# Optimization experiments

Hardware: AMD Instinct MI355X
Metric: run time of the kernel (lower is better)

## Reference

```python
import jax, jax.numpy as jnp
import numpy as np

N = 200_000           # particles
E = 6_400_000         # neighbor pairs (~32 per particle)
SUPPORT = 0.05
EPS = SUPPORT ** 2 * 0.1
DELTA = 0.1
C0 = 10.0 * float(np.sqrt(2.0 * 9.81 * 0.3))
REST_DENSITY = 1000.0
_KC = 7.0 / float(np.pi)  # 2D Wendland C2 normalization


def kernel_gradient(q, dirs, h):
    # Wendland C2 (2D): W = C/h^2 (1-q)^4 (1+4q), q = r/h in [0,1]
    # dW/dr = C/h^3 * (-20 q (1-q)^3), directed along unit vector dirs
    dkdq = -20.0 * q * (1.0 - q) ** 3 * _KC
    return dirs * (dkdq / h ** 3)[:, None]


def setup_inputs() -> dict:
    key = jax.random.key(0)
    k = jax.random.split(key, 7)
    i = jnp.sort(jax.random.randint(k[0], (E,), 0, N))
    j = jax.random.randint(k[1], (E,), 0, N)
    fluidPosition = jax.random.uniform(k[2], (N, 2), dtype=jnp.float32)
    dx2 = (SUPPORT * 0.5) ** 2
    fluidVolume = dx2 * (1.0 + 0.01 * jax.random.normal(k[3], (N,), dtype=jnp.float32))
    fluidDensity = 0.95 + 0.1 * jax.random.uniform(k[4], (N,), dtype=jnp.float32)
    d = jax.random.normal(k[5], (E, 2), dtype=jnp.float32)
    distances = d / (jnp.linalg.norm(d, axis=1, keepdims=True) + 1e-8)  # unit directions
    radialDistances = jax.random.uniform(k[6], (E,), dtype=jnp.float32, minval=0.05, maxval=1.0)
    return {"fluidPosition": fluidPosition, "fluidVolume": fluidVolume,
            "fluidDensity": fluidDensity, "distances": distances,
            "radialDistances": radialDistances, "i": i, "j": j}


def reference(fluidPosition, fluidVolume, fluidDensity, distances, radialDistances, i, j):
    h = SUPPORT
    n = fluidDensity.shape[0]
    gradW = kernel_gradient(radialDistances, distances, h)          # [E,2]
    r_ba = -distances * (radialDistances * h)[:, None]              # [E,2] displacement
    Vj = fluidVolume[j]

    # --- normalization matrix: sum_j 2 Vj * outer(r_ba, gradW) ---
    term = jnp.einsum('nu,nv->nuv', r_ba, gradW) * (2.0 * Vj)[:, None, None]
    M = jax.ops.segment_sum(term, i, num_segments=n)                # [N,2,2]

    # --- pseudo-inverse + renormalized kernel gradient per edge ---
    Li = jnp.linalg.pinv(M)                                         # [N,2,2]
    grad = jnp.einsum('nuv,nv->nu', Li[i], gradW)                   # [E,2]
    dwij_mag = jnp.sum(jnp.abs(gradW), axis=1)                      # L1 norms
    norm_mag = jnp.sum(jnp.abs(grad), axis=1)
    change = jnp.abs(norm_mag - dwij_mag) / (dwij_mag + 1e-4 * h)
    grad = jnp.where((change < 0.1)[:, None], grad, gradW)

    # --- renormalized density gradient ---
    rho = fluidDensity * REST_DENSITY
    rho_ba = rho[j] - rho[i]
    gradRho = jax.ops.segment_sum((2.0 * rho_ba * Vj)[:, None] * grad, i, num_segments=n)

    # --- deltaSPH density diffusion ---
    rji2 = jnp.sum(r_ba * r_ba, axis=1) + EPS
    densityTerm = 0.5 * jnp.einsum('nu,nu->n', gradRho[i] + gradRho[j], r_ba)
    gradTerm = jnp.einsum('nu,nu->n', gradW, r_ba / rji2[:, None])
    prod = (rho_ba + densityTerm) * gradTerm
    return 2.0 * h * DELTA * C0 * jax.ops.segment_sum(prod * Vj, i, num_segments=n)
```

## Files before the change

### kernel.cpp

```cpp
#include <hip/hip_runtime.h>
#include <hip/hip_fp16.h>
#include <math.h>

#define WAVE   64
#define NPB    32
#define BLOCKT 256
#define SMAX   2

#define KC        2.2281692032865347f
#define H         0.05f
#define INV_H2    400.0f
#define INV_H3    8000.0f
#define EPS_REF   0.00025f
#define K_OUT     0.24261080f
#define REST_RHO  1000.0f

__device__ __forceinline__ float wendland_dkdq(float q) {
    float o = 1.f - q;
    return -20.f * q * o * o * o * KC;
}

union H2F { __half2 h; float f; };
__device__ __forceinline__ float   h2_as_f(__half2 h) { H2F u; u.h = h; return u.f; }
__device__ __forceinline__ __half2 f_as_h2(float f)   { H2F u; u.f = f; return u.h; }

__device__ __forceinline__ int li_search(const int* rp, int e) {
    int lo = 0;
#pragma unroll
    for (int s = NPB / 2; s >= 1; s >>= 1) lo += (rp[lo + s] <= e) ? s : 0;
    return lo;
}

template<int NV>
__device__ __forceinline__ void seg_reduce4(const int k[4], float v[4][NV], float* base) {
    const int lane = threadIdx.x & (WAVE - 1);
    const int k0 = k[0], k3 = k[3];
    const bool split = (k0 != k3);
    const int firstLen  = (k[1]==k0) ? ((k[2]==k0) ? ((k[3]==k0)?4:3) : 2) : 1;
    const int lastStart = (k[2]==k3) ? ((k[1]==k3) ? ((k[0]==k3)?0:1) : 2) : 3;

    float vin[NV], vfirst[NV];
#pragma unroll
    for (int c = 0; c < NV; ++c) {
        float s = v[3][c];
        if (lastStart <= 2) s += v[2][c];
        if (lastStart <= 1) s += v[1][c];
        if (lastStart == 0) s += v[0][c];
        vin[c] = s;
        float f = v[0][c];
        if (firstLen >= 2) f += v[1][c];
        if (firstLen >= 3) f += v[2][c];
        if (firstLen >= 4) f += v[3][c];
        vfirst[c] = f;
    }
#pragma unroll
    for (int idx = 1; idx <= 2; ++idx) {
        if (idx >= firstLen && idx < lastStart && k[idx] >= 0) {
#pragma unroll
            for (int c = 0; c < NV; ++c)
                atomicAdd(base + (size_t)k[idx] * NV + c, v[idx][c]);
        }
    }
    float S[NV];
#pragma unroll
    for (int c = 0; c < NV; ++c) S[c] = vin[c];
    const int klast = k3;
#pragma unroll
    for (int d = 1; d < WAVE; d <<= 1) {
        int okey = __shfl_up(klast, d, WAVE);
        float ov[NV];
#pragma unroll
        for (int c = 0; c < NV; ++c) ov[c] = __shfl_up(S[c], d, WAVE);
        if (lane >= d && okey == klast) {
#pragma unroll
            for (int c = 0; c < NV; ++c) S[c] += ov[c];
        }
    }
    const int prevk = __shfl_up(klast, 1, WAVE);
    float P[NV];
#pragma unroll
    for (int c = 0; c < NV; ++c) P[c] = __shfl_up(S[c], 1, WAVE);
    if (split && k0 >= 0) {
        const bool carry = (lane > 0 && prevk == k0);
#pragma unroll
        for (int c = 0; c < NV; ++c)
            atomicAdd(base + (size_t)k0 * NV + c, vfirst[c] + (carry ? P[c] : 0.f));
    }
    const int nk0 = __shfl_down(k0, 1, WAVE);
    const bool tail = (lane == WAVE - 1) || (nk0 != klast);
    if (tail && klast >= 0) {
#pragma unroll
        for (int c = 0; c < NV; ++c)
            atomicAdd(base + (size_t)klast * NV + c, S[c]);
    }
}

struct EW { int jv[4]; float qv[4], dxv[4], dyv[4]; bool okv[4]; };

__device__ __forceinline__ void load_win(long e0, int beg, int end, int E,
        const int* __restrict__ ej, const float* __restrict__ qarr,
        const float2* __restrict__ dirs, EW& w) {
    if (e0 + 3 < (long)E) {
        int4   j4 = *(const int4*)(ej + e0);
        float4 q4 = *(const float4*)(qarr + e0);
        float4 dA = *(const float4*)((const float*)dirs + 2 * e0);
        float4 dB = *(const float4*)((const float*)dirs + 2 * e0 + 4);
        w.jv[0]=j4.x; w.jv[1]=j4.y; w.jv[2]=j4.z; w.jv[3]=j4.w;
        w.qv[0]=q4.x; w.qv[1]=q4.y; w.qv[2]=q4.z; w.qv[3]=q4.w;
        w.dxv[0]=dA.x; w.dyv[0]=dA.y; w.dxv[1]=dA.z; w.dyv[1]=dA.w;
        w.dxv[2]=dB.x; w.dyv[2]=dB.y; w.dxv[3]=dB.z; w.dyv[3]=dB.w;
    } else {
#pragma unroll
        for (int u = 0; u < 4; ++u) {
            long e = e0 + u;
            if (e < (long)E) {
                w.jv[u] = ej[e]; w.qv[u] = qarr[e];
                float2 d = dirs[e]; w.dxv[u] = d.x; w.dyv[u] = d.y;
            } else { w.jv[u]=0; w.qv[u]=0.f; w.dxv[u]=0.f; w.dyv[u]=0.f; }
        }
    }
#pragma unroll
    for (int u = 0; u < 4; ++u) {
        long e = e0 + u;
        w.okv[u] = (e >= (long)beg) && (e < (long)end);
    }
}

__global__ void k_prep(const int* __restrict__ ei, const float* __restrict__ vol,
                       const float* __restrict__ dens, int* __restrict__ rowptr,
                       float2* __restrict__ vd, int N, int E) {
    int e = blockIdx.x * blockDim.x + threadIdx.x;
    if (e <= E) {
        int prev = (e == 0) ? -1 : ei[e - 1];
        int cur  = (e == E) ? N  : ei[e];
        for (int t = prev + 1; t <= cur; ++t) rowptr[t] = e;
    }
    if (e < N) vd[e] = make_float2(vol[e], dens[e]);
}

__global__ __launch_bounds__(BLOCKT, 4)
void k_AC(const int* __restrict__ ej, const float* __restrict__ qarr,
          const float2* __restrict__ dirs, const float2* __restrict__ vd,
          const int* __restrict__ rowptr, __half2* __restrict__ cst,
          float2* __restrict__ g2, float* __restrict__ outp, int N, int E) {
    __shared__ int    rp[NPB + 1];
    __shared__ float  acc6[NPB * 6];
    __shared__ float  Lild[NPB * 3];
    __shared__ float  gld[NPB * 2];
    __shared__ float2 vdl[NPB];
    const int tid = threadIdx.x;
    const int n0  = blockIdx.x * NPB;
    const int nHi = min(n0 + NPB, N);
    if (tid <= NPB) rp[tid] = rowptr[min(n0 + tid, nHi)];
    if (tid < NPB && n0 + tid < N) vdl[tid] = vd[n0 + tid];
    if (tid < NPB * 6) acc6[tid] = 0.f;
    if (tid < NPB * 2) gld[tid] = 0.f;
    __syncthreads();
    const int  beg = rp[0], end = rp[NPB];
    const long beg4 = (long)beg & ~3L;
    const int  waveBase = tid & ~(WAVE - 1);

    int   li_s[4 * SMAX];
    float w_s[4 * SMAX], dx_s[4 * SMAX], dy_s[4 * SMAX], val_s[4 * SMAX];
#pragma unroll
    for (int x = 0; x < 4 * SMAX; ++x) { li_s[x] = -1; w_s[x]=dx_s[x]=dy_s[x]=val_s[x]=0.f; }

#pragma unroll
    for (int c = 0; c < SMAX; ++c) {
        long ebw = beg4 + ((long)c * BLOCKT + waveBase) * 4;
        if (ebw < (long)end) {
            long e0 = beg4 + ((long)c * BLOCKT + tid) * 4;
            EW wd; load_win(e0, beg, end, E, ej, qarr, dirs, wd);
            const bool all4 = wd.okv[0] && wd.okv[1] && wd.okv[2] && wd.okv[3];
            float4 cpack;
            int k[4]; float v[4][6];
#pragma unroll
            for (int u = 0; u < 4; ++u) {
                k[u] = -1;
#pragma unroll
                for (int c2 = 0; c2 < 6; ++c2) v[u][c2] = 0.f;
                if (wd.okv[u]) {
                    int li = li_search(rp, (int)(e0 + u));
                    float q = wd.qv[u], dx = wd.dxv[u], dy = wd.dyv[u];
                    float2 vdj = vd[wd.jv[u]];
                    float wq = wendland_dkdq(q);
                    float s = -2.f * vdj.x * q * wq * INV_H2;
                    float w = wq * INV_H3;
                    float gwx = dx * w, gwy = dy * w;
                    float rx = -dx * q * H, ry = -dy * q * H;
                    float rji2 = rx * rx + ry * ry + EPS_REF;
                    float gT = (gwx * rx + gwy * ry) / rji2;
                    float gv = gT * vdj.x;
                    float rho_ba = REST_RHO * (vdj.y - vdl[li].y);
                    k[u] = li;
                    v[u][0] = s * dx * dx; v[u][1] = s * dx * dy; v[u][2] = s * dy * dy;
                    v[u][3] = rho_ba * gv; v[u][4] = rx * gv;    v[u][5] = ry * gv;
                    __half2 cp = __floats2half2_rn(0.5f * rx * gv, 0.5f * ry * gv);
                    if (all4) (&cpack.x)[u] = h2_as_f(cp);
                    else      cst[e0 + u] = cp;
                    li_s[c*4+u] = li; w_s[c*4+u] = w;
                    dx_s[c*4+u] = dx; dy_s[c*4+u] = dy;
                    val_s[c*4+u] = 2.f * rho_ba * vdj.x;
                }
            }
            if (all4) ((float4*)cst)[e0 >> 2] = cpack;
            seg_reduce4<6>(k, v, acc6);
        }
    }
    for (int c = SMAX; ; ++c) {
        long ebw = beg4 + ((long)c * BLOCKT + waveBase) * 4;
        if (ebw >= (long)end) break;
        long e0 = beg4 + ((long)c * BLOCKT + tid) * 4;
        EW wd; load_win(e0, beg, end, E, ej, qarr, dirs, wd);
        int k[4]; float v[4][6];
#pragma unroll
        for (int u = 0; u < 4; ++u) {
            k[u] = -1;
#pragma unroll
            for (int c2 = 0; c2 < 6; ++c2) v[u][c2] = 0.f;
            if (wd.okv[u]) {
                int li = li_search(rp, (int)(e0 + u));
                float q = wd.qv[u], dx = wd.dxv[u], dy = wd.dyv[u];
                float2 vdj = vd[wd.jv[u]];
                float wq = wendland_dkdq(q);
                float s = -2.f * vdj.x * q * wq * INV_H2;
                float w = wq * INV_H3;
                float gwx = dx * w, gwy = dy * w;
                float rx = -dx * q * H, ry = -dy * q * H;
                float rji2 = rx * rx + ry * ry + EPS_REF;
                float gT = (gwx * rx + gwy * ry) / rji2;
                float gv = gT * vdj.x;
                float rho_ba = REST_RHO * (vdj.y - vdl[li].y);
                k[u] = li;
                v[u][0] = s * dx * dx; v[u][1] = s * dx * dy; v[u][2] = s * dy * dy;
                v[u][3] = rho_ba * gv; v[u][4] = rx * gv;    v[u][5] = ry * gv;
                cst[e0 + u] = __floats2half2_rn(0.5f * rx * gv, 0.5f * ry * gv);
            }
        }
        seg_reduce4<6>(k, v, acc6);
    }
    __syncthreads();

    if (tid < NPB) {
        float a = acc6[6*tid], b = acc6[6*tid+1], cc = acc6[6*tid+2];
        float half_tr   = 0.5f * (a + cc);
        float half_diff = 0.5f * (a - cc);
        float disc = sqrtf(half_diff * half_diff + b * b);
        float l1 = half_tr + disc, l2 = half_tr - disc;
        float smax = fmaxf(fabsf(l1), fabsf(l2));
        float cutoff = 2.3841858e-6f * smax;
        float i00 = 0.f, i01 = 0.f, i11 = 0.f;
        if (fabsf(l2) > cutoff) {
            float inv = 1.0f / (a * cc - b * b);
            i00 =  cc * inv; i01 = -b * inv; i11 = a * inv;
        } else if (fabsf(l1) > cutoff) {
            float vax = b,       vay = l1 - a;
            float vbx = l1 - cc, vby = b;
            float na = vax*vax + vay*vay, nb = vbx*vbx + vby*vby;
            float vx, vy, n2;
            if (nb >= na) { vx = vbx; vy = vby; n2 = nb; }
            else          { vx = vax; vy = vay; n2 = na; }
            float inv = 1.0f / (l1 * n2);
            i00 = vx*vx*inv; i01 = vx*vy*inv; i11 = vy*vy*inv;
        }
        Lild[3*tid] = i00; Lild[3*tid+1] = i01; Lild[3*tid+2] = i11;
    }
    __syncthreads();

#pragma unroll
    for (int c = 0; c < SMAX; ++c) {
        long ebw = beg4 + ((long)c * BLOCKT + waveBase) * 4;
        if (ebw < (long)end) {
            int k[4]; float v[4][2];
#pragma unroll
            for (int u = 0; u < 4; ++u) {
                int li = li_s[c*4+u];
                k[u] = li; v[u][0] = v[u][1] = 0.f;
                if (li >= 0) {
                    float w = w_s[c*4+u], dx = dx_s[c*4+u], dy = dy_s[c*4+u];
                    float gwx = dx * w, gwy = dy * w;
                    float L0 = Lild[3*li], L1 = Lild[3*li+1], L2v = Lild[3*li+2];
                    float gx = L0 * gwx + L1 * gwy;
                    float gy = L1 * gwx + L2v * gwy;
                    float dm = fabsf(gwx) + fabsf(gwy);
                    float nm = fabsf(gx) + fabsf(gy);
                    float change = fabsf(nm - dm) / (dm + 1e-4f * H);
                    if (!(change < 0.1f)) { gx = gwx; gy = gwy; }
                    v[u][0] = val_s[c*4+u] * gx;
                    v[u][1] = val_s[c*4+u] * gy;
                }
            }
            seg_reduce4<2>(k, v, gld);
        }
    }
    for (int c = SMAX; ; ++c) {
        long ebw = beg4 + ((long)c * BLOCKT + waveBase) * 4;
        if (ebw >= (long)end) break;
        long e0 = beg4 + ((long)c * BLOCKT + tid) * 4;
        EW wd; load_win(e0, beg, end, E, ej, qarr, dirs, wd);
        int k[4]; float v[4][2];
#pragma unroll
        for (int u = 0; u < 4; ++u) {
            k[u] = -1; v[u][0] = v[u][1] = 0.f;
            if (wd.okv[u]) {
                int li = li_search(rp, (int)(e0 + u));
                float q = wd.qv[u], dx = wd.dxv[u], dy = wd.dyv[u];
                float2 vdj = vd[wd.jv[u]];
                float w = wendland_dkdq(q) * INV_H3;
                float gwx = dx * w, gwy = dy * w;
                float L0 = Lild[3*li], L1 = Lild[3*li+1], L2v = Lild[3*li+2];
                float gx = L0 * gwx + L1 * gwy;
                float gy = L1 * gwx + L2v * gwy;
                float dm = fabsf(gwx) + fabsf(gwy);
                float nm = fabsf(gx) + fabsf(gy);
                float change = fabsf(nm - dm) / (dm + 1e-4f * H);
                if (!(change < 0.1f)) { gx = gwx; gy = gwy; }
                float val = 2.f * REST_RHO * (vdj.y - vdl[li].y) * vdj.x;
                k[u] = li; v[u][0] = val * gx; v[u][1] = val * gy;
            }
        }
        seg_reduce4<2>(k, v, gld);
    }
    __syncthreads();
    if (tid < NPB && n0 + tid < N) {
        float gx = gld[2*tid], gy = gld[2*tid+1];
        g2[n0 + tid]   = make_float2(gx, gy);
        outp[n0 + tid] = acc6[6*tid+3] + 0.5f * (gx * acc6[6*tid+4] + gy * acc6[6*tid+5]);
    }
}

__global__ __launch_bounds__(BLOCKT, 4)
void k_D(const int* __restrict__ ej, const __half2* __restrict__ cst,
         const float2* __restrict__ g2, const float* __restrict__ outp,
         const int* __restrict__ rowptr, float* __restrict__ out, int N, int E) {
    __shared__ int   rp[NPB + 1];
    __shared__ float outl[NPB];
    const int tid = threadIdx.x;
    const int n0  = blockIdx.x * NPB;
    const int nHi = min(n0 + NPB, N);
    if (tid <= NPB) rp[tid] = rowptr[min(n0 + tid, nHi)];
    if (tid < NPB) outl[tid] = 0.f;
    __syncthreads();
    const int  beg = rp[0], end = rp[NPB];
    const long beg4 = (long)beg & ~3L;
    const int  waveBase = tid & ~(WAVE - 1);

    for (int c = 0; ; ++c) {
        long ebw = beg4 + ((long)c * BLOCKT + waveBase) * 4;
        if (ebw >= (long)end) break;
        long e0 = beg4 + ((long)c * BLOCKT + tid) * 4;
        int jv[4]; float cv[4]; bool okv[4];
        if (e0 + 3 < (long)E) {
            int4   j4 = *(const int4*)(ej + e0);
            float4 c4 = ((const float4*)cst)[e0 >> 2];
            jv[0]=j4.x; jv[1]=j4.y; jv[2]=j4.z; jv[3]=j4.w;
            cv[0]=c4.x; cv[1]=c4.y; cv[2]=c4.z; cv[3]=c4.w;
        } else {
#pragma unroll
            for (int u = 0; u < 4; ++u) {
                long e = e0 + u;
                if (e < (long)E) { jv[u] = ej[e]; cv[u] = h2_as_f(cst[e]); }
                else             { jv[u] = 0;     cv[u] = 0.f; }
            }
        }
#pragma unroll
        for (int u = 0; u < 4; ++u) {
            long e = e0 + u;
            okv[u] = (e >= (long)beg) && (e < (long)end);
        }
        int k[4]; float v[4][1];
#pragma unroll
        for (int u = 0; u < 4; ++u) {
            k[u] = -1; v[u][0] = 0.f;
            if (okv[u]) {
                int li = li_search(rp, (int)(e0 + u));
                float2 gj = g2[jv[u]];
                __half2 ch = f_as_h2(cv[u]);
                k[u] = li;
                v[u][0] = gj.x * __low2float(ch) + gj.y * __high2float(ch);
            }
        }
        seg_reduce4<1>(k, v, outl);
    }
    __syncthreads();
    if (tid < NPB && n0 + tid < N)
        out[n0 + tid] = K_OUT * (outp[n0 + tid] + outl[tid]);
}

extern "C" void kernel_launch(void* const* d_in, const int* in_sizes, int n_in,
                              void* d_out, int out_size, void* d_ws, size_t ws_size,
                              hipStream_t stream) {
    const float*  vol  = (const float*)d_in[1];
    const float*  dens = (const float*)d_in[2];
    const float2* dirs = (const float2*)d_in[3];
    const float*  qarr = (const float*)d_in[4];
    const int*    ei   = (const int*)d_in[5];
    const int*    ej   = (const int*)d_in[6];
    const int N = in_sizes[1];
    const int E = in_sizes[4];

    size_t off = 0;
    auto alloc = [&](size_t bytes) { void* r = (char*)d_ws + off;
                                     off = (off + bytes + 15) & ~(size_t)15; return r; };
    int*     rowptr = (int*)    alloc((size_t)(N + 1) * 4);
    float2*  vd     = (float2*) alloc((size_t)N * 8);
    float2*  g2     = (float2*) alloc((size_t)N * 8);
    float*   outp   = (float*)  alloc((size_t)N * 4);
    __half2* cst    = (__half2*)alloc((size_t)E * 4);
    float*   out    = (float*)d_out;

    const int tb = 256;
    const int gP = (E + 1 + tb - 1) / tb;
    const int gB = (N + NPB - 1) / NPB;

    k_prep<<<gP, tb, 0, stream>>>(ei, vol, dens, rowptr, vd, N, E);
    k_AC  <<<gB, BLOCKT, 0, stream>>>(ej, qarr, dirs, vd, rowptr, cst, g2, outp, N, E);
    k_D   <<<gB, BLOCKT, 0, stream>>>(ej, cst, g2, outp, rowptr, out, N, E);
}
```

Measured before the change: 245.5 us.

## Shrink blocks to one wave with fewer nodes per block and cache gradient

Each block now handles 16 particles with a single 64-thread wavefront instead of 32 particles with 256 threads. The register cache also holds three stages instead of two, and it stores the precomputed gradW components rather than w, dx and dy. Smaller blocks are meant to cut idle lanes and imbalance when a segment has few edges, and the per-wave loop condition becomes a block-wide condition. The trade-off is more blocks, fewer threads to amortise shared-memory setup and syncs per block, and higher register pressure from the larger cache.

```diff
diff --git a/kernel.cpp b/kernel.cpp
--- a/kernel.cpp
+++ b/kernel.cpp
@@ -3,9 +3,9 @@
 #include <math.h>
 
 #define WAVE   64
-#define NPB    32
-#define BLOCKT 256
-#define SMAX   2
+#define NPB    16
+#define BLOCKT 64
+#define SMAX   3
 
 #define KC        2.2281692032865347f
 #define H         0.05f
@@ -138,7 +138,7 @@
     if (e < N) vd[e] = make_float2(vol[e], dens[e]);
 }
 
-__global__ __launch_bounds__(BLOCKT, 4)
+__global__ __launch_bounds__(BLOCKT)
 void k_AC(const int* __restrict__ ej, const float* __restrict__ qarr,
           const float2* __restrict__ dirs, const float2* __restrict__ vd,
           const int* __restrict__ rowptr, __half2* __restrict__ cst,
@@ -153,21 +153,20 @@
     const int nHi = min(n0 + NPB, N);
     if (tid <= NPB) rp[tid] = rowptr[min(n0 + tid, nHi)];
     if (tid < NPB && n0 + tid < N) vdl[tid] = vd[n0 + tid];
-    if (tid < NPB * 6) acc6[tid] = 0.f;
+    for (int x = tid; x < NPB * 6; x += BLOCKT) acc6[x] = 0.f;
     if (tid < NPB * 2) gld[tid] = 0.f;
     __syncthreads();
     const int  beg = rp[0], end = rp[NPB];
     const long beg4 = (long)beg & ~3L;
-    const int  waveBase = tid & ~(WAVE - 1);
 
     int   li_s[4 * SMAX];
-    float w_s[4 * SMAX], dx_s[4 * SMAX], dy_s[4 * SMAX], val_s[4 * SMAX];
-#pragma unroll
-    for (int x = 0; x < 4 * SMAX; ++x) { li_s[x] = -1; w_s[x]=dx_s[x]=dy_s[x]=val_s[x]=0.f; }
+    float gwx_s[4 * SMAX], gwy_s[4 * SMAX], val_s[4 * SMAX];
+#pragma unroll
+    for (int x = 0; x < 4 * SMAX; ++x) { li_s[x] = -1; gwx_s[x]=gwy_s[x]=val_s[x]=0.f; }
 
 #pragma unroll
     for (int c = 0; c < SMAX; ++c) {
-        long ebw = beg4 + ((long)c * BLOCKT + waveBase) * 4;
+        long ebw = beg4 + (long)c * BLOCKT * 4;
         if (ebw < (long)end) {
             long e0 = beg4 + ((long)c * BLOCKT + tid) * 4;
             EW wd; load_win(e0, beg, end, E, ej, qarr, dirs, wd);
@@ -198,8 +197,7 @@
                     __half2 cp = __floats2half2_rn(0.5f * rx * gv, 0.5f * ry * gv);
                     if (all4) (&cpack.x)[u] = h2_as_f(cp);
                     else      cst[e0 + u] = cp;
-                    li_s[c*4+u] = li; w_s[c*4+u] = w;
-                    dx_s[c*4+u] = dx; dy_s[c*4+u] = dy;
+                    li_s[c*4+u] = li; gwx_s[c*4+u] = gwx; gwy_s[c*4+u] = gwy;
                     val_s[c*4+u] = 2.f * rho_ba * vdj.x;
                 }
             }
@@ -208,7 +206,7 @@
         }
     }
     for (int c = SMAX; ; ++c) {
-        long ebw = beg4 + ((long)c * BLOCKT + waveBase) * 4;
+        long ebw = beg4 + (long)c * BLOCKT * 4;
         if (ebw >= (long)end) break;
         long e0 = beg4 + ((long)c * BLOCKT + tid) * 4;
         EW wd; load_win(e0, beg, end, E, ej, qarr, dirs, wd);
@@ -269,7 +267,7 @@
 
 #pragma unroll
     for (int c = 0; c < SMAX; ++c) {
-        long ebw = beg4 + ((long)c * BLOCKT + waveBase) * 4;
+        long ebw = beg4 + (long)c * BLOCKT * 4;
         if (ebw < (long)end) {
             int k[4]; float v[4][2];
 #pragma unroll
@@ -277,8 +275,7 @@
                 int li = li_s[c*4+u];
                 k[u] = li; v[u][0] = v[u][1] = 0.f;
                 if (li >= 0) {
-                    float w = w_s[c*4+u], dx = dx_s[c*4+u], dy = dy_s[c*4+u];
-                    float gwx = dx * w, gwy = dy * w;
+                    float gwx = gwx_s[c*4+u], gwy = gwy_s[c*4+u];
                     float L0 = Lild[3*li], L1 = Lild[3*li+1], L2v = Lild[3*li+2];
                     float gx = L0 * gwx + L1 * gwy;
                     float gy = L1 * gwx + L2v * gwy;
@@ -294,7 +291,7 @@
         }
     }
     for (int c = SMAX; ; ++c) {
-        long ebw = beg4 + ((long)c * BLOCKT + waveBase) * 4;
+        long ebw = beg4 + (long)c * BLOCKT * 4;
         if (ebw >= (long)end) break;
         long e0 = beg4 + ((long)c * BLOCKT + tid) * 4;
         EW wd; load_win(e0, beg, end, E, ej, qarr, dirs, wd);
@@ -329,7 +326,7 @@
     }
 }
 
-__global__ __launch_bounds__(BLOCKT, 4)
+__global__ __launch_bounds__(BLOCKT)
 void k_D(const int* __restrict__ ej, const __half2* __restrict__ cst,
          const float2* __restrict__ g2, const float* __restrict__ outp,
          const int* __restrict__ rowptr, float* __restrict__ out, int N, int E) {
@@ -343,13 +340,12 @@
     __syncthreads();
     const int  beg = rp[0], end = rp[NPB];
     const long beg4 = (long)beg & ~3L;
-    const int  waveBase = tid & ~(WAVE - 1);
 
     for (int c = 0; ; ++c) {
-        long ebw = beg4 + ((long)c * BLOCKT + waveBase) * 4;
+        long ebw = beg4 + (long)c * BLOCKT * 4;
         if (ebw >= (long)end) break;
         long e0 = beg4 + ((long)c * BLOCKT + tid) * 4;
-        int jv[4]; float cv[4]; bool okv[4];
+        int jv[4]; float cv[4];
         if (e0 + 3 < (long)E) {
             int4   j4 = *(const int4*)(ej + e0);
             float4 c4 = ((const float4*)cst)[e0 >> 2];
@@ -363,17 +359,13 @@
                 else             { jv[u] = 0;     cv[u] = 0.f; }
             }
         }
+        int k[4]; float v[4][1];
 #pragma unroll
         for (int u = 0; u < 4; ++u) {
             long e = e0 + u;
-            okv[u] = (e >= (long)beg) && (e < (long)end);
-        }
-        int k[4]; float v[4][1];
-#pragma unroll
-        for (int u = 0; u < 4; ++u) {
             k[u] = -1; v[u][0] = 0.f;
-            if (okv[u]) {
-                int li = li_search(rp, (int)(e0 + u));
+            if (e >= (long)beg && e < (long)end) {
+                int li = li_search(rp, (int)e);
                 float2 gj = g2[jv[u]];
                 __half2 ch = f_as_h2(cv[u]);
                 k[u] = li;
```

Result: no change. 248.2 us (+1.1%).
